# Kernel tuning notes

Hardware: AMD Instinct MI355X
Metric: run time of the kernel (lower is better)

## Reference

```python
import jax, jax.numpy as jnp
import numpy as np
import math

B, S, D = 2, 2048, 1024
H, KV, HD = 16, 4, 64
G = H // KV          # kv groups
CAP = 50.0           # attention soft-cap
EPS = 1e-6           # RMSNorm eps


def _rmsnorm(x, w):
    return x * jax.lax.rsqrt(jnp.mean(x * x, axis=-1, keepdims=True) + EPS) * w


def _rope(x, freqs):
    # x: (b, h, s, hd); freqs: (S, hd//2, 2) with [...,0]=cos, [...,1]=sin
    s = x.shape[2]
    xp = x.reshape(*x.shape[:-1], -1, 2)
    cos = freqs[:s, :, 0][None, None]   # (1,1,s,hd//2)
    sin = freqs[:s, :, 1][None, None]
    x0, x1 = xp[..., 0], xp[..., 1]
    out = jnp.stack([x0 * cos - x1 * sin, x0 * sin + x1 * cos], axis=-1)
    return out.reshape(x.shape)


def setup_inputs() -> dict:
    key = jax.random.key(0)
    ks = jax.random.split(key, 6)
    x = jax.random.normal(ks[0], (B, S, D), dtype=jnp.float32)
    # realistic RoPE table: theta_i = pos / 10000^(2i/hd)
    inv_freq = 1.0 / (10000.0 ** (np.arange(0, HD, 2, dtype=np.float32) / HD))
    theta = np.arange(S, dtype=np.float32)[:, None] * inv_freq[None, :]
    rope_freqs = jnp.asarray(np.stack([np.cos(theta), np.sin(theta)], axis=-1))
    sc = 0.02
    wq = jax.random.normal(ks[1], (2 * H * HD, D), dtype=jnp.float32) * sc
    wk = jax.random.normal(ks[2], (2 * KV * HD, D), dtype=jnp.float32) * sc
    wv = jax.random.normal(ks[3], (KV * HD, D), dtype=jnp.float32) * sc
    wo = jax.random.normal(ks[4], (D, H * HD), dtype=jnp.float32) * sc
    q_norm_w = jnp.ones((HD,), dtype=jnp.float32)
    k_norm_w = jnp.ones((HD,), dtype=jnp.float32)
    diff_lambda = jnp.array([0.8], dtype=jnp.float32)
    return {"x": x, "rope_freqs": rope_freqs, "wq": wq, "wk": wk, "wv": wv,
            "wo": wo, "q_norm_w": q_norm_w, "k_norm_w": k_norm_w,
            "diff_lambda": diff_lambda}


def reference(x, rope_freqs, wq, wk, wv, wo, q_norm_w, k_norm_w, diff_lambda):
    b, s, _ = x.shape
    # projections (torch Linear: y = x @ W^T)
    q = (x @ wq.T).reshape(b, s, H, 2 * HD).transpose(0, 2, 1, 3)   # (b,H,s,2hd)
    k = (x @ wk.T).reshape(b, s, KV, 2 * HD).transpose(0, 2, 1, 3)  # (b,KV,s,2hd)
    v = (x @ wv.T).reshape(b, s, KV, HD).transpose(0, 2, 1, 3)      # (b,KV,s,hd)
    q1, q2 = jnp.split(q, 2, axis=-1)
    k1, k2 = jnp.split(k, 2, axis=-1)
    # QK-norm (before RoPE, as in the torch module)
    q1, q2 = _rmsnorm(q1, q_norm_w), _rmsnorm(q2, q_norm_w)
    k1, k2 = _rmsnorm(k1, k_norm_w), _rmsnorm(k2, k_norm_w)
    # RoPE
    q1, q2 = _rope(q1, rope_freqs), _rope(q2, rope_freqs)
    k1, k2 = _rope(k1, rope_freqs), _rope(k2, rope_freqs)
    # GQA expansion: each kv head repeated G times contiguously
    k1 = jnp.repeat(k1, G, axis=1)
    k2 = jnp.repeat(k2, G, axis=1)
    v = jnp.repeat(v, G, axis=1)
    scale = 1.0 / math.sqrt(HD)
    scores1 = jnp.einsum('bhqd,bhkd->bhqk', q1, k1) * scale
    scores2 = jnp.einsum('bhqd,bhkd->bhqk', q2, k2) * scale
    # soft-cap
    scores1 = CAP * jnp.tanh(scores1 / CAP)
    scores2 = CAP * jnp.tanh(scores2 / CAP)
    mask = jnp.triu(jnp.full((s, s), -jnp.inf, dtype=scores1.dtype), 1)
    attn1 = jax.nn.softmax(scores1 + mask, axis=-1)
    attn2 = jax.nn.softmax(scores2 + mask, axis=-1)
    diff_attn = attn1 - diff_lambda[0] * attn2
    out = jnp.einsum('bhqk,bhkd->bhqd', diff_attn, v)
    out = out.transpose(0, 2, 1, 3).reshape(b, s, H * HD)
    return out @ wo.T
```

## Files before the change

### kernel.cpp

```cpp
#include <hip/hip_runtime.h>
#include <hip/hip_bf16.h>

#define B_ 2
#define S_ 2048
#define D_ 1024
#define H_ 16
#define KV_ 4
#define HD_ 64
#define G_ (H_ / KV_)
#define NCAT 2816
#define VOFF 2560

typedef __attribute__((ext_vector_type(8))) short short8;
typedef __attribute__((ext_vector_type(4))) short short4v;
typedef __attribute__((ext_vector_type(2))) int int2v;
typedef __attribute__((ext_vector_type(4))) int int4v;
typedef __attribute__((ext_vector_type(4))) float floatx4;

using gvoid_p = const __attribute__((address_space(1))) void*;
using lvoid_p = __attribute__((address_space(3))) void*;

__device__ inline void gload_lds16(const short* g, short* l) {
    __builtin_amdgcn_global_load_lds((gvoid_p)(const void*)g, (lvoid_p)(void*)l, 16, 0, 0);
}

__device__ inline int cvt_pk_bf16(float lo, float hi) {
    int r;
    asm volatile("v_cvt_pk_bf16_f32 %0, %1, %2" : "=v"(r) : "v"(lo), "v"(hi));
    return r;
}

__device__ inline float bf16lo(unsigned u) {
    return __builtin_bit_cast(float, u << 16);
}
__device__ inline float bf16hi(unsigned u) {
    return __builtin_bit_cast(float, u & 0xffff0000u);
}

__global__ void cvt5_kernel(const float* s0, const float* s1, const float* s2,
                            const float* s3, const float* s4,
                            __hip_bfloat16* d0, __hip_bfloat16* d1, __hip_bfloat16* d2,
                            __hip_bfloat16* d3, __hip_bfloat16* d4,
                            int n0, int n1, int n2, int n3, int n4) {
    const float* s; __hip_bfloat16* d; int n;
    switch (blockIdx.y) {
        case 0: s = s0; d = d0; n = n0; break;
        case 1: s = s1; d = d1; n = n1; break;
        case 2: s = s2; d = d2; n = n2; break;
        case 3: s = s3; d = d3; n = n3; break;
        default: s = s4; d = d4; n = n4; break;
    }
    int nv = n >> 2;
    for (int i = blockIdx.x * blockDim.x + threadIdx.x; i < nv;
         i += gridDim.x * blockDim.x) {
        floatx4 v = ((const floatx4*)s)[i];
        short4v o;
#pragma unroll
        for (int e = 0; e < 4; ++e) {
            __hip_bfloat16 hh = __float2bfloat16(v[e]);
            o[e] = __builtin_bit_cast(short, hh);
        }
        ((short4v*)d)[i] = o;
    }
}

template <typename OutT>
__global__ __launch_bounds__(256) void gemm_bt_lds(const short* __restrict__ A,
                                                   const short* __restrict__ Bm,
                                                   OutT* __restrict__ C,
                                                   int M, int N, int K) {
    __shared__ __align__(16) short As[2][128 * 32];
    __shared__ __align__(16) short Bs[2][128 * 32];
    int tid = threadIdx.x;
    int wid = tid >> 6, lane = tid & 63;
    int wr = wid >> 1, wc = wid & 1;
    int r = lane & 15, kq = lane >> 4;

    int nwg = gridDim.x * gridDim.y;
    int orig = blockIdx.y * gridDim.x + blockIdx.x;
    int wg = (orig & 7) * (nwg >> 3) + (orig >> 3);
    int bx = wg % gridDim.x, by = wg / gridDim.x;

    long m0 = (long)by * 128;
    long n0 = (long)bx * 128;

    const short* gA0 = A + (m0 + (tid >> 2)) * (long)K + (tid & 3) * 8;
    const short* gA1 = A + (m0 + 64 + (tid >> 2)) * (long)K + (tid & 3) * 8;
    const short* gB0 = Bm + (n0 + (tid >> 2)) * (long)K + (tid & 3) * 8;
    const short* gB1 = Bm + (n0 + 64 + (tid >> 2)) * (long)K + (tid & 3) * 8;

    auto stage = [&](int buf, int k0) {
        gload_lds16(gA0 + k0, &As[buf][wid * 512]);
        gload_lds16(gA1 + k0, &As[buf][2048 + wid * 512]);
        gload_lds16(gB0 + k0, &Bs[buf][wid * 512]);
        gload_lds16(gB1 + k0, &Bs[buf][2048 + wid * 512]);
    };

    floatx4 acc[4][4];
#pragma unroll
    for (int i = 0; i < 4; ++i)
#pragma unroll
        for (int j = 0; j < 4; ++j) acc[i][j] = {0.f, 0.f, 0.f, 0.f};

    int nt = K >> 5;
    stage(0, 0);
    for (int t = 0; t < nt; ++t) {
        int cur = t & 1;
        __builtin_amdgcn_s_barrier();
        if (t + 1 < nt) {
            stage(cur ^ 1, (t + 1) << 5);
            asm volatile("s_waitcnt vmcnt(4)" ::: "memory");
        } else {
            asm volatile("s_waitcnt vmcnt(0)" ::: "memory");
        }
        __builtin_amdgcn_sched_barrier(0);
        __builtin_amdgcn_s_barrier();
        short8 a[4], b[4];
#pragma unroll
        for (int mi = 0; mi < 4; ++mi)
            a[mi] = *(const short8*)&As[cur][(wr * 64 + mi * 16 + r) * 32 + kq * 8];
#pragma unroll
        for (int ni = 0; ni < 4; ++ni)
            b[ni] = *(const short8*)&Bs[cur][(wc * 64 + ni * 16 + r) * 32 + kq * 8];
#pragma unroll
        for (int mi = 0; mi < 4; ++mi)
#pragma unroll
            for (int ni = 0; ni < 4; ++ni)
                acc[mi][ni] = __builtin_amdgcn_mfma_f32_16x16x32_bf16(
                    a[mi], b[ni], acc[mi][ni], 0, 0, 0);
    }
    int col_l = lane & 15, row_l = (lane >> 4) * 4;
#pragma unroll
    for (int mi = 0; mi < 4; ++mi)
#pragma unroll
        for (int ni = 0; ni < 4; ++ni) {
            long col = n0 + wc * 64 + ni * 16 + col_l;
            long row0 = m0 + wr * 64 + mi * 16 + row_l;
#pragma unroll
            for (int j = 0; j < 4; ++j) {
                float v = acc[mi][ni][j];
                if constexpr (__is_same(OutT, float))
                    C[(row0 + j) * N + col] = v;
                else
                    C[(row0 + j) * N + col] = __float2bfloat16(v);
            }
        }
}

__global__ void norm_rope_kernel(const __hip_bfloat16* __restrict__ buf,
                                 __hip_bfloat16* __restrict__ outb,
                                 const float* __restrict__ freqs,
                                 const float* __restrict__ w, int nvec, int nh,
                                 int tstride, int colbase) {
    int gt = blockIdx.x * blockDim.x + threadIdx.x;
    int gw = gt >> 6;
    int lane = gt & 63;
    if (gw >= nvec) return;
    int t = gw / (nh * 2);
    int rem = gw - t * (nh * 2);
    int s = t & (S_ - 1);
    const __hip_bfloat16* v = buf + (long)t * tstride + colbase + rem * 64;
    float x = __bfloat162float(v[lane]);
    float ss = x * x;
#pragma unroll
    for (int off = 32; off; off >>= 1) ss += __shfl_xor(ss, off);
    float r = rsqrtf(ss * (1.f / 64.f) + 1e-6f);
    x = x * r * w[lane];
    int i = lane >> 1;
    float c  = freqs[(s * (HD_ / 2) + i) * 2];
    float sn = freqs[(s * (HD_ / 2) + i) * 2 + 1];
    float p = __shfl_xor(x, 1);
    float y = (lane & 1) ? fmaf(p, sn, x * c) : fmaf(x, c, -(p * sn));
    outb[(long)gw * 64 + lane] = __float2bfloat16(y);
}

__global__ __launch_bounds__(256) void v_transpose_kernel(const short* __restrict__ src,
                                                          short* __restrict__ dst) {
    __shared__ short ls[64][72];
    int s0 = blockIdx.x * 64;
    int kv = blockIdx.y, b = blockIdx.z;
    int tid = threadIdx.x;
    const short* base = src + ((long)(b * S_ + s0)) * NCAT + VOFF + kv * 64;
    {
        int rr = tid >> 2, cc = (tid & 3) * 16;
        *(short8*)&ls[rr][cc]     = *(const short8*)(base + (long)rr * NCAT + cc);
        *(short8*)&ls[rr][cc + 8] = *(const short8*)(base + (long)rr * NCAT + cc + 8);
    }
    __syncthreads();
    short* ob = dst + ((long)(b * KV_ + kv) * 64) * S_ + s0;
    {
        int d = tid >> 2, sl = (tid & 3) * 16;
        short8 o0, o1;
#pragma unroll
        for (int e = 0; e < 8; ++e) { o0[e] = ls[sl + e][d]; o1[e] = ls[sl + 8 + e][d]; }
        *(short8*)(ob + (long)d * S_ + sl)     = o0;
        *(short8*)(ob + (long)d * S_ + sl + 8) = o1;
    }
}

__global__ __launch_bounds__(256, 4) void attn_kernel(const short* __restrict__ qb,
                                                      const short* __restrict__ kbuf,
                                                      const short* __restrict__ vtb,
                                                      __hip_bfloat16* __restrict__ ob,
                                                      unsigned* __restrict__ part,
                                                      float* __restrict__ lpart,
                                                      const float* __restrict__ lam_p) {
    __shared__ __align__(16) short Ks[3][32][128];
    __shared__ __align__(16) short Vt[2][64][40];

    int tid = threadIdx.x, w = tid >> 6, lane = tid & 63;
    int raw = (int)blockIdx.x;
    int xcd = raw & 7;
    int kv = xcd & 3, b = xcd >> 2;
    int i5 = raw >> 3;
    int x = i5 & 31, hh = i5 >> 5;
    int h = kv * G_ + hh;
    int p = x >> 1, e = x & 1;
    int qtA = p, qtB = 31 - p;
    int r = lane & 15, kq = lane >> 4;
    float lam = lam_p[0];

    floatx4 acc[2][4];
    floatx4 accl[2];
    short8 qa[2][2];

    const short* vbase = vtb + (long)(b * KV_ + kv) * 64 * S_;
    const float c1 = 0.18033688f, nc4 = -3.7570e-7f, zoff = -17.3123405f;
    const short one_bf = (short)0x3F80;
    short8 ones8 = {one_bf, one_bf, one_bf, one_bf, one_bf, one_bf, one_bf, one_bf};

    int ch1 = tid + 256;
    int krow0 = tid >> 4, kcs0 = ((tid & 15) ^ (krow0 & 7)) * 8;
    int krow1 = ch1 >> 4, kcs1 = ((ch1 & 15) ^ (krow1 & 7)) * 8;
    const short* kgb = kbuf + ((long)b * S_ * KV_ + kv) * 128;
    int vd = tid >> 2, vch = tid & 3;

    auto issueK = [&](int buf, int ki) {
        long rb = (long)(ki * 32) * (KV_ * 128);
        gload_lds16(kgb + rb + (long)krow0 * (KV_ * 128) + kcs0, &Ks[buf][0][0] + w * 512);
        gload_lds16(kgb + rb + (long)krow1 * (KV_ * 128) + kcs1, &Ks[buf][0][0] + 2048 + w * 512);
    };
    auto loadV = [&](int kb) {
        return *(const short8*)(vbase + (long)vd * S_ + kb + vch * 8);
    };

    auto reset_acc = [&]() {
#pragma unroll
        for (int m = 0; m < 2; ++m) {
            accl[m] = {0.f, 0.f, 0.f, 0.f};
#pragma unroll
            for (int dt = 0; dt < 4; ++dt) acc[m][dt] = {0.f, 0.f, 0.f, 0.f};
        }
    };
    auto load_q = [&](int q0) {
        const short* qrow = qb + ((long)(b * S_ + q0 + r) * H_ + h) * 128;
        qa[0][0] = *(const short8*)(qrow + kq * 8);
        qa[0][1] = *(const short8*)(qrow + 32 + kq * 8);
        qa[1][0] = *(const short8*)(qrow + 64 + kq * 8);
        qa[1][1] = *(const short8*)(qrow + 96 + kq * 8);
    };

    auto tile_compute = [&](int bk, int cv, int kb, int q0, bool domask) {
        int rel = q0 + r - kb;
        short8 vb[4];
#pragma unroll
        for (int dt = 0; dt < 4; ++dt) {
            const short* vrow = &Vt[cv][dt * 16 + r][0];
            int2v lo = *(const int2v*)(vrow + 4 * kq);
            int2v hi = *(const int2v*)(vrow + 16 + 4 * kq);
            vb[dt] = __builtin_bit_cast(short8, int4v{lo[0], lo[1], hi[0], hi[1]});
        }
#pragma unroll
        for (int m = 0; m < 2; ++m) {
            floatx4 sacc[2];
            __builtin_amdgcn_s_setprio(1);
#pragma unroll
            for (int nt = 0; nt < 2; ++nt) {
                sacc[nt] = {0.f, 0.f, 0.f, 0.f};
                const short* row = &Ks[bk][nt * 16 + r][0];
                short8 a0 = *(const short8*)(row + (((m * 8) + kq) ^ (r & 7)) * 8);
                short8 a1 = *(const short8*)(row + (((m * 8) + 4 + kq) ^ (r & 7)) * 8);
                sacc[nt] = __builtin_amdgcn_mfma_f32_16x16x32_bf16(a0, qa[m][0], sacc[nt], 0, 0, 0);
                sacc[nt] = __builtin_amdgcn_mfma_f32_16x16x32_bf16(a1, qa[m][1], sacc[nt], 0, 0, 0);
            }
            __builtin_amdgcn_s_setprio(0);
            float pv[2][4];
#pragma unroll
            for (int nt = 0; nt < 2; ++nt)
#pragma unroll
                for (int j = 0; j < 4; ++j) {
                    float rawv = sacc[nt][j];
                    float r2 = rawv * rawv;
                    float z = fmaf(rawv, fmaf(r2, nc4, c1), zoff);
                    pv[nt][j] = __builtin_amdgcn_exp2f(z);
                }
            if (domask) {
#pragma unroll
                for (int nt = 0; nt < 2; ++nt)
#pragma unroll
                    for (int j = 0; j < 4; ++j)
                        if (nt * 16 + kq * 4 + j > rel) pv[nt][j] = 0.f;
            }
            int d0 = cvt_pk_bf16(pv[0][0], pv[0][1]);
            int d1 = cvt_pk_bf16(pv[0][2], pv[0][3]);
            int d2 = cvt_pk_bf16(pv[1][0], pv[1][1]);
            int d3 = cvt_pk_bf16(pv[1][2], pv[1][3]);
            short8 pa8 = __builtin_bit_cast(short8, int4v{d0, d1, d2, d3});
            __builtin_amdgcn_s_setprio(1);
#pragma unroll
            for (int dt = 0; dt < 4; ++dt)
                acc[m][dt] = __builtin_amdgcn_mfma_f32_16x16x32_bf16(
                    pa8, vb[dt], acc[m][dt], 0, 0, 0);
            accl[m] = __builtin_amdgcn_mfma_f32_16x16x32_bf16(pa8, ones8, accl[m], 0, 0, 0);
            __builtin_amdgcn_s_setprio(0);
        }
    };

    auto run = [&](int qt, int ki0, int ki1, bool diag) {
        int q0 = qt * 64 + w * 16;
        load_q(q0);
        reset_acc();
        int nseg = ki1 - ki0;
        issueK(0, ki0);
        short8 rva = loadV(ki0 * 32), rvb;
        int bk = 0;
        for (int ii = 0; ii < nseg; ++ii) {
            int ki = ki0 + ii, cv = ii & 1;
            bool pre = (ii + 1 < nseg);
            int bk1 = (bk == 2) ? 0 : bk + 1;
            if (pre) issueK(bk1, ki + 1);
            if (pre) asm volatile("s_waitcnt vmcnt(2)" ::: "memory");
            else     asm volatile("s_waitcnt vmcnt(0)" ::: "memory");
            __builtin_amdgcn_sched_barrier(0);
            if (cv == 0) {
                *(short8*)&Vt[0][vd][vch * 8] = rva;
                if (pre) rvb = loadV((ki + 1) * 32);
            } else {
                *(short8*)&Vt[1][vd][vch * 8] = rvb;
                if (pre) rva = loadV((ki + 1) * 32);
            }
            asm volatile("s_waitcnt lgkmcnt(0)" ::: "memory");
            __builtin_amdgcn_sched_barrier(0);
            __builtin_amdgcn_s_barrier();
            tile_compute(bk, cv, ki * 32, q0, diag && ((ki >> 1) == qt));
            bk = bk1;
        }
        __builtin_amdgcn_s_barrier();
    };

    if (e == 0) {
        run(qtA, 0, 2 * qtA + 2, true);
        {
            int q0 = qtA * 64 + w * 16;
#pragma unroll
            for (int j = 0; j < 4; ++j) {
                float i1 = 1.f / accl[0][j];
                float i2 = lam / accl[1][j];
                int qr = q0 + kq * 4 + j;
                __hip_bfloat16* orow = ob + ((long)(b * S_ + qr) * H_ + h) * 64;
#pragma unroll
                for (int dt = 0; dt < 4; ++dt) {
                    float val = acc[0][dt][j] * i1 - acc[1][dt][j] * i2;
                    orow[dt * 16 + r] = __float2bfloat16(val);
                }
            }
        }
        run(qtB, 0, 31 - 2 * p, false);
    } else {
        run(qtB, 31 - 2 * p, 64 - 2 * p, true);
    }

    {
        long slot = (long)(b * H_ + h) * 16 + (qtB - 16);
        long base = (slot * 2 + e) * 4096L;
        int qloc = w * 16 + kq * 4;
#pragma unroll
        for (int dt = 0; dt < 4; ++dt)
#pragma unroll
            for (int j = 0; j < 4; ++j)
                part[base + (qloc + j) * 64 + dt * 16 + r] =
                    (unsigned)cvt_pk_bf16(acc[0][dt][j], acc[1][dt][j]);
        if (r == 0) {
#pragma unroll
            for (int m = 0; m < 2; ++m)
#pragma unroll
                for (int j = 0; j < 4; ++j)
                    lpart[((slot * 2 + e) * 2 + m) * 64 + qloc + j] = accl[m][j];
        }
    }
}

__global__ __launch_bounds__(256) void attn_merge_kernel(const unsigned* __restrict__ part,
                                                         const float* __restrict__ lpart,
                                                         __hip_bfloat16* __restrict__ ob,
                                                         const float* __restrict__ lam_p) {
    long sid = blockIdx.x;
    int t16 = sid & 15;
    int h = (sid >> 4) & (H_ - 1);
    int b = (int)(sid >> 8);
    int qt = 16 + t16;
    float lam = lam_p[0];
    const unsigned* p0 = part + sid * 2 * 4096L;
    const unsigned* p1 = part + (sid * 2 + 1) * 4096L;
    const float* l0 = lpart + sid * 4 * 64L;
    const float* l1 = lpart + (sid * 4 + 2) * 64L;
    int tid = threadIdx.x;
#pragma unroll
    for (int i = 0; i < 16; ++i) {
        int idx = i * 256 + tid;
        int q = idx >> 6, d = idx & 63;
        unsigned u0 = p0[q * 64 + d], u1 = p1[q * 64 + d];
        float a1 = bf16lo(u0) + bf16lo(u1);
        float a2 = bf16hi(u0) + bf16hi(u1);
        float L1 = l0[q] + l1[q];
        float L2 = l0[64 + q] + l1[64 + q];
        float val = a1 / L1 - lam * (a2 / L2);
        ob[((long)(b * S_ + qt * 64 + q) * H_ + h) * 64 + d] = __float2bfloat16(val);
    }
}

extern "C" void kernel_launch(void* const* d_in, const int* in_sizes, int n_in,
                              void* d_out, int out_size, void* d_ws, size_t ws_size,
                              hipStream_t stream) {
    const float* x     = (const float*)d_in[0];
    const float* freqs = (const float*)d_in[1];
    const float* wq    = (const float*)d_in[2];
    const float* wk    = (const float*)d_in[3];
    const float* wv    = (const float*)d_in[4];
    const float* wo    = (const float*)d_in[5];
    const float* qnw   = (const float*)d_in[6];
    const float* knw   = (const float*)d_in[7];
    const float* lam   = (const float*)d_in[8];
    float* out = (float*)d_out;

    const int T = B_ * S_;
    char* ws = (char*)d_ws;
    size_t off = 0;
    auto alloc = [&](size_t bytes) {
        void* p = ws + off;
        off += (bytes + 255) & ~(size_t)255;
        return p;
    };
    __hip_bfloat16* xb   = (__hip_bfloat16*)alloc((size_t)T * D_ * 2);
    __hip_bfloat16* wcat = (__hip_bfloat16*)alloc((size_t)NCAT * D_ * 2);
    __hip_bfloat16* wob  = (__hip_bfloat16*)alloc((size_t)D_ * D_ * 2);
    __hip_bfloat16* qkvb = (__hip_bfloat16*)alloc((size_t)T * NCAT * 2);
    __hip_bfloat16* qb16 = (__hip_bfloat16*)alloc((size_t)T * 2 * H_ * HD_ * 2);
    __hip_bfloat16* kb16 = (__hip_bfloat16*)alloc((size_t)T * 2 * KV_ * HD_ * 2);
    __hip_bfloat16* vT   = (__hip_bfloat16*)alloc((size_t)B_ * KV_ * HD_ * S_ * 2);
    unsigned* part = (unsigned*)alloc((size_t)512 * 2 * 4096 * 4);
    float* lpart   = (float*)alloc((size_t)512 * 2 * 2 * 64 * 4);
    __hip_bfloat16* aob  = xb;

    cvt5_kernel<<<dim3(2048, 5), 256, 0, stream>>>(
        x, wq, wk, wv, wo,
        xb, wcat, wcat + (size_t)2 * H_ * HD_ * D_,
        wcat + (size_t)(2 * H_ * HD_ + 2 * KV_ * HD_) * D_, wob,
        T * D_, 2 * H_ * HD_ * D_, 2 * KV_ * HD_ * D_, KV_ * HD_ * D_, D_ * D_);

    gemm_bt_lds<__hip_bfloat16><<<dim3(NCAT / 128, T / 128), 256, 0, stream>>>(
        (const short*)xb, (const short*)wcat, qkvb, T, NCAT, D_);

    {
        int nvq = T * H_ * 2;
        norm_rope_kernel<<<(nvq * 64 + 255) / 256, 256, 0, stream>>>(
            qkvb, qb16, freqs, qnw, nvq, H_, NCAT, 0);
        int nvk = T * KV_ * 2;
        norm_rope_kernel<<<(nvk * 64 + 255) / 256, 256, 0, stream>>>(
            qkvb, kb16, freqs, knw, nvk, KV_, NCAT, 2 * H_ * HD_);
        v_transpose_kernel<<<dim3(S_ / 64, KV_, B_), 256, 0, stream>>>(
            (const short*)qkvb, (short*)vT);
    }

    attn_kernel<<<1024, 256, 0, stream>>>(
        (const short*)qb16, (const short*)kb16, (const short*)vT, aob, part, lpart, lam);
    attn_merge_kernel<<<512, 256, 0, stream>>>(part, lpart, aob, lam);

    gemm_bt_lds<float><<<dim3(D_ / 128, T / 128), 256, 0, stream>>>(
        (const short*)aob, (const short*)wob, out, T, D_, D_);
}
```

Baseline: 171.5 us.

## Fuse QK RMSNorm, RoPE and V transpose into QKV projection GEMM epilogue

Replaces the QKV GEMM, two norm_rope launches and the V transpose kernel with one GEMM whose epilogue applies RMSNorm and RoPE to Q/K tiles in registers via lane shuffles, and writes V directly in transposed layout. This removes the intermediate qkv buffer round trip through memory and three kernel launches. In exchange the epilogue does strided, uncoalesced stores for V (stride S per element) and per-element freq loads, which may cost bandwidth. Numerics also change slightly because the norm is computed on fp32 accumulators instead of bf16-rounded values.

```diff
diff --git a/kernel.cpp b/kernel.cpp
--- a/kernel.cpp
+++ b/kernel.cpp
@@ -64,6 +64,134 @@
     }
 }
 
+__global__ __launch_bounds__(256) void gemm_qkv_fused(const short* __restrict__ A,
+                                                      const short* __restrict__ Bm,
+                                                      __hip_bfloat16* __restrict__ qout,
+                                                      __hip_bfloat16* __restrict__ kout,
+                                                      __hip_bfloat16* __restrict__ vout,
+                                                      const float* __restrict__ freqs,
+                                                      const float* __restrict__ qnw,
+                                                      const float* __restrict__ knw,
+                                                      int M, int N, int K) {
+    __shared__ __align__(16) short As[2][128 * 32];
+    __shared__ __align__(16) short Bs[2][128 * 32];
+    int tid = threadIdx.x;
+    int wid = tid >> 6, lane = tid & 63;
+    int wr = wid >> 1, wc = wid & 1;
+    int r = lane & 15, kq = lane >> 4;
+
+    int nwg = gridDim.x * gridDim.y;
+    int orig = blockIdx.y * gridDim.x + blockIdx.x;
+    int wg = (orig & 7) * (nwg >> 3) + (orig >> 3);
+    int bx = wg % gridDim.x, by = wg / gridDim.x;
+
+    long m0 = (long)by * 128;
+    long n0 = (long)bx * 128;
+
+    const short* gA0 = A + (m0 + (tid >> 2)) * (long)K + (tid & 3) * 8;
+    const short* gA1 = A + (m0 + 64 + (tid >> 2)) * (long)K + (tid & 3) * 8;
+    const short* gB0 = Bm + (n0 + (tid >> 2)) * (long)K + (tid & 3) * 8;
+    const short* gB1 = Bm + (n0 + 64 + (tid >> 2)) * (long)K + (tid & 3) * 8;
+
+    auto stage = [&](int buf, int k0) {
+        gload_lds16(gA0 + k0, &As[buf][wid * 512]);
+        gload_lds16(gA1 + k0, &As[buf][2048 + wid * 512]);
+        gload_lds16(gB0 + k0, &Bs[buf][wid * 512]);
+        gload_lds16(gB1 + k0, &Bs[buf][2048 + wid * 512]);
+    };
+
+    floatx4 acc[4][4];
+#pragma unroll
+    for (int i = 0; i < 4; ++i)
+#pragma unroll
+        for (int j = 0; j < 4; ++j) acc[i][j] = {0.f, 0.f, 0.f, 0.f};
+
+    int nt = K >> 5;
+    stage(0, 0);
+    for (int t = 0; t < nt; ++t) {
+        int cur = t & 1;
+        __builtin_amdgcn_s_barrier();
+        if (t + 1 < nt) {
+            stage(cur ^ 1, (t + 1) << 5);
+            asm volatile("s_waitcnt vmcnt(4)" ::: "memory");
+        } else {
+            asm volatile("s_waitcnt vmcnt(0)" ::: "memory");
+        }
+        __builtin_amdgcn_sched_barrier(0);
+        __builtin_amdgcn_s_barrier();
+        short8 a[4], b[4];
+#pragma unroll
+        for (int mi = 0; mi < 4; ++mi)
+            a[mi] = *(const short8*)&As[cur][(wr * 64 + mi * 16 + r) * 32 + kq * 8];
+#pragma unroll
+        for (int ni = 0; ni < 4; ++ni)
+            b[ni] = *(const short8*)&Bs[cur][(wc * 64 + ni * 16 + r) * 32 + kq * 8];
+#pragma unroll
+        for (int mi = 0; mi < 4; ++mi)
+#pragma unroll
+            for (int ni = 0; ni < 4; ++ni)
+                acc[mi][ni] = __builtin_amdgcn_mfma_f32_16x16x32_bf16(
+                    a[mi], b[ni], acc[mi][ni], 0, 0, 0);
+    }
+
+    int col_l = lane & 15;
+    int gbase = (int)n0 + wc * 64;
+    int par = col_l & 1;
+    if (gbase < VOFF) {
+        const float* wnorm = (gbase < 2048) ? qnw : knw;
+        float wv4[4];
+        int fo[4];
+#pragma unroll
+        for (int ni = 0; ni < 4; ++ni) {
+            wv4[ni] = wnorm[ni * 16 + col_l];
+            fo[ni] = ni * 16 + (col_l >> 1) * 2;
+        }
+        __hip_bfloat16* outp;
+        long tstride;
+        int cbase;
+        if (gbase < 2048) { outp = qout; tstride = 2048; cbase = gbase; }
+        else              { outp = kout; tstride = 512;  cbase = gbase - 2048; }
+#pragma unroll
+        for (int mi = 0; mi < 4; ++mi) {
+#pragma unroll
+            for (int j = 0; j < 4; ++j) {
+                int t = (int)m0 + wr * 64 + mi * 16 + kq * 4 + j;
+                float ss = 0.f;
+#pragma unroll
+                for (int ni = 0; ni < 4; ++ni)
+                    ss = fmaf(acc[mi][ni][j], acc[mi][ni][j], ss);
+                ss += __shfl_xor(ss, 1); ss += __shfl_xor(ss, 2);
+                ss += __shfl_xor(ss, 4); ss += __shfl_xor(ss, 8);
+                float rr = rsqrtf(ss * (1.f / 64.f) + 1e-6f);
+                const float* fb = freqs + (long)(t & (S_ - 1)) * 64;
+                __hip_bfloat16* orow = outp + (long)t * tstride + cbase;
+#pragma unroll
+                for (int ni = 0; ni < 4; ++ni) {
+                    float xv = acc[mi][ni][j] * rr * wv4[ni];
+                    float pp = __shfl_xor(xv, 1);
+                    float cc = fb[fo[ni]], sn = fb[fo[ni] + 1];
+                    float y = par ? fmaf(pp, sn, xv * cc) : fmaf(xv, cc, -(pp * sn));
+                    orow[ni * 16 + col_l] = __float2bfloat16(y);
+                }
+            }
+        }
+    } else {
+        int kvv = (gbase - VOFF) >> 6;
+#pragma unroll
+        for (int mi = 0; mi < 4; ++mi) {
+#pragma unroll
+            for (int j = 0; j < 4; ++j) {
+                int t = (int)m0 + wr * 64 + mi * 16 + kq * 4 + j;
+                int bb = t >> 11, st = t & (S_ - 1);
+                __hip_bfloat16* vcol = vout + ((long)(bb * KV_ + kvv) * 64) * S_ + st;
+#pragma unroll
+                for (int ni = 0; ni < 4; ++ni)
+                    vcol[(long)(ni * 16 + col_l) * S_] = __float2bfloat16(acc[mi][ni][j]);
+            }
+        }
+    }
+}
+
 template <typename OutT>
 __global__ __launch_bounds__(256) void gemm_bt_lds(const short* __restrict__ A,
                                                    const short* __restrict__ Bm,
@@ -145,57 +273,6 @@
                     C[(row0 + j) * N + col] = __float2bfloat16(v);
             }
         }
-}
-
-__global__ void norm_rope_kernel(const __hip_bfloat16* __restrict__ buf,
-                                 __hip_bfloat16* __restrict__ outb,
-                                 const float* __restrict__ freqs,
-                                 const float* __restrict__ w, int nvec, int nh,
-                                 int tstride, int colbase) {
-    int gt = blockIdx.x * blockDim.x + threadIdx.x;
-    int gw = gt >> 6;
-    int lane = gt & 63;
-    if (gw >= nvec) return;
-    int t = gw / (nh * 2);
-    int rem = gw - t * (nh * 2);
-    int s = t & (S_ - 1);
-    const __hip_bfloat16* v = buf + (long)t * tstride + colbase + rem * 64;
-    float x = __bfloat162float(v[lane]);
-    float ss = x * x;
-#pragma unroll
-    for (int off = 32; off; off >>= 1) ss += __shfl_xor(ss, off);
-    float r = rsqrtf(ss * (1.f / 64.f) + 1e-6f);
-    x = x * r * w[lane];
-    int i = lane >> 1;
-    float c  = freqs[(s * (HD_ / 2) + i) * 2];
-    float sn = freqs[(s * (HD_ / 2) + i) * 2 + 1];
-    float p = __shfl_xor(x, 1);
-    float y = (lane & 1) ? fmaf(p, sn, x * c) : fmaf(x, c, -(p * sn));
-    outb[(long)gw * 64 + lane] = __float2bfloat16(y);
-}
-
-__global__ __launch_bounds__(256) void v_transpose_kernel(const short* __restrict__ src,
-                                                          short* __restrict__ dst) {
-    __shared__ short ls[64][72];
-    int s0 = blockIdx.x * 64;
-    int kv = blockIdx.y, b = blockIdx.z;
-    int tid = threadIdx.x;
-    const short* base = src + ((long)(b * S_ + s0)) * NCAT + VOFF + kv * 64;
-    {
-        int rr = tid >> 2, cc = (tid & 3) * 16;
-        *(short8*)&ls[rr][cc]     = *(const short8*)(base + (long)rr * NCAT + cc);
-        *(short8*)&ls[rr][cc + 8] = *(const short8*)(base + (long)rr * NCAT + cc + 8);
-    }
-    __syncthreads();
-    short* ob = dst + ((long)(b * KV_ + kv) * 64) * S_ + s0;
-    {
-        int d = tid >> 2, sl = (tid & 3) * 16;
-        short8 o0, o1;
-#pragma unroll
-        for (int e = 0; e < 8; ++e) { o0[e] = ls[sl + e][d]; o1[e] = ls[sl + 8 + e][d]; }
-        *(short8*)(ob + (long)d * S_ + sl)     = o0;
-        *(short8*)(ob + (long)d * S_ + sl + 8) = o1;
-    }
 }
 
 __global__ __launch_bounds__(256, 4) void attn_kernel(const short* __restrict__ qb,
@@ -444,7 +521,6 @@
     __hip_bfloat16* xb   = (__hip_bfloat16*)alloc((size_t)T * D_ * 2);
     __hip_bfloat16* wcat = (__hip_bfloat16*)alloc((size_t)NCAT * D_ * 2);
     __hip_bfloat16* wob  = (__hip_bfloat16*)alloc((size_t)D_ * D_ * 2);
-    __hip_bfloat16* qkvb = (__hip_bfloat16*)alloc((size_t)T * NCAT * 2);
     __hip_bfloat16* qb16 = (__hip_bfloat16*)alloc((size_t)T * 2 * H_ * HD_ * 2);
     __hip_bfloat16* kb16 = (__hip_bfloat16*)alloc((size_t)T * 2 * KV_ * HD_ * 2);
     __hip_bfloat16* vT   = (__hip_bfloat16*)alloc((size_t)B_ * KV_ * HD_ * S_ * 2);
@@ -458,19 +534,9 @@
         wcat + (size_t)(2 * H_ * HD_ + 2 * KV_ * HD_) * D_, wob,
         T * D_, 2 * H_ * HD_ * D_, 2 * KV_ * HD_ * D_, KV_ * HD_ * D_, D_ * D_);
 
-    gemm_bt_lds<__hip_bfloat16><<<dim3(NCAT / 128, T / 128), 256, 0, stream>>>(
-        (const short*)xb, (const short*)wcat, qkvb, T, NCAT, D_);
-
-    {
-        int nvq = T * H_ * 2;
-        norm_rope_kernel<<<(nvq * 64 + 255) / 256, 256, 0, stream>>>(
-            qkvb, qb16, freqs, qnw, nvq, H_, NCAT, 0);
-        int nvk = T * KV_ * 2;
-        norm_rope_kernel<<<(nvk * 64 + 255) / 256, 256, 0, stream>>>(
-            qkvb, kb16, freqs, knw, nvk, KV_, NCAT, 2 * H_ * HD_);
-        v_transpose_kernel<<<dim3(S_ / 64, KV_, B_), 256, 0, stream>>>(
-            (const short*)qkvb, (short*)vT);
-    }
+    gemm_qkv_fused<<<dim3(NCAT / 128, T / 128), 256, 0, stream>>>(
+        (const short*)xb, (const short*)wcat, qb16, kb16, vT,
+        freqs, qnw, knw, T, NCAT, D_);
 
     attn_kernel<<<1024, 256, 0, stream>>>(
         (const short*)qb16, (const short*)kb16, (const short*)vT, aob, part, lpart, lam);
```

Result: faster. 162.2 us (-5.4%).
